# Optimization experiments

Measured on AMD Instinct MI355X. Metric: run time of the kernel, lower is better.

Reference implementation:

```python
import jax, jax.numpy as jnp
import numpy as np

SOFTCAP = 50.0  # GEMMA2_TANH_SCALE
N_HEADS = 16

def _rope(x, cos, sin):
    # x: [B,S,H,D]; cos/sin: [S,D/2]; interleaved complex pairs as in apply_rotary_emb
    x0 = x[..., 0::2]
    x1 = x[..., 1::2]
    c = cos[None, :, None, :]
    s = sin[None, :, None, :]
    r0 = x0 * c - x1 * s
    r1 = x0 * s + x1 * c
    return jnp.stack([r0, r1], axis=-1).reshape(x.shape)

def setup_inputs() -> dict:
    key = jax.random.key(0)
    ks = jax.random.split(key, 5)
    B, S, DM = 1, 2048, 2048
    hd = DM // N_HEADS
    scale = 1.0 / np.sqrt(DM)
    x = jax.random.normal(ks[0], (B, S, DM), jnp.float32)
    wq = jax.random.normal(ks[1], (DM, DM), jnp.float32) * scale
    wk = jax.random.normal(ks[2], (DM, DM), jnp.float32) * scale
    wv = jax.random.normal(ks[3], (DM, DM), jnp.float32) * scale
    wo = jax.random.normal(ks[4], (DM, DM), jnp.float32) * scale
    # rotary tables, theta=10000 as in llama
    inv_freq = 10000.0 ** (-jnp.arange(0, hd, 2, dtype=jnp.float32) / hd)
    ang = jnp.arange(S, dtype=jnp.float32)[:, None] * inv_freq[None, :]
    return {"x": x, "wq": wq, "wk": wk, "wv": wv, "wo": wo,
            "freqs_cos": jnp.cos(ang), "freqs_sin": jnp.sin(ang)}

def reference(x, wq, wk, wv, wo, freqs_cos, freqs_sin):
    B, S, DM = x.shape
    H = N_HEADS
    hd = DM // H
    q = (x @ wq).reshape(B, S, H, hd)
    k = (x @ wk).reshape(B, S, H, hd)
    v = (x @ wv).reshape(B, S, H, hd)
    q = _rope(q, freqs_cos, freqs_sin)
    k = _rope(k, freqs_cos, freqs_sin)
    # scores [B,H,S,S]
    scores = jnp.einsum('bqhd,bkhd->bhqk', q, k) / jnp.sqrt(jnp.float32(hd))
    scores = SOFTCAP * jnp.tanh(scores / SOFTCAP)  # gemma2 tanh soft-cap
    causal = jnp.tril(jnp.ones((S, S), dtype=bool))
    scores = jnp.where(causal[None, None], scores, -jnp.inf)
    p = jax.nn.softmax(scores, axis=-1)
    o = jnp.einsum('bhqk,bkhd->bqhd', p, v).reshape(B, S, DM)
    return o @ wo
```

## Files before the change

### kernel.cpp

```cpp
#include <hip/hip_runtime.h>
#include <hip/hip_bf16.h>

typedef __attribute__((ext_vector_type(8))) short short8;
typedef __attribute__((ext_vector_type(4))) short short4v;
typedef __attribute__((ext_vector_type(4))) float f32x4;
typedef __attribute__((ext_vector_type(4))) float float4v;

#define S_LEN 2048
#define DMODEL 2048
#define N_HEADS 16
#define HEAD_DIM 128

__device__ __forceinline__ float bf2f(__hip_bfloat16 b) { return __bfloat162float(b); }
__device__ __forceinline__ __hip_bfloat16 f2bf(float f) { return __float2bfloat16(f); }
__device__ __forceinline__ short bfs(float f) {
    union { __hip_bfloat16 b; short s; } x; x.b = __float2bfloat16(f); return x.s;
}
__device__ __forceinline__ float sbf(short s) {
    union { short s; __hip_bfloat16 b; } x; x.s = s; return __bfloat162float(x.b);
}

#if __has_builtin(__builtin_amdgcn_global_load_lds)
#define HAVE_ASYNC_LDS 1
#else
#define HAVE_ASYNC_LDS 0
#endif

__device__ __forceinline__ void stage16(const __hip_bfloat16* g, __hip_bfloat16* ldsbase, int lane) {
#if HAVE_ASYNC_LDS
    __builtin_amdgcn_global_load_lds(
        (const __attribute__((address_space(1))) unsigned int*)g,
        (__attribute__((address_space(3))) unsigned int*)ldsbase,
        16, 0, 0);
#else
    *(short8*)((char*)ldsbase + lane * 16) = *(const short8*)g;
#endif
}

__global__ __launch_bounds__(256) void prep(const float* __restrict__ x,
                                            const float* __restrict__ w0,
                                            const float* __restrict__ w1,
                                            const float* __restrict__ w2,
                                            const float* __restrict__ w3,
                                            __hip_bfloat16* __restrict__ xb,
                                            __hip_bfloat16* __restrict__ o0,
                                            __hip_bfloat16* __restrict__ o1,
                                            __hip_bfloat16* __restrict__ o2,
                                            __hip_bfloat16* __restrict__ o3) {
    const int z = blockIdx.z;
    const int tid = threadIdx.x;
    if (z == 4) {
        size_t base = (((size_t)blockIdx.y * 32 + blockIdx.x) * 256 + tid) * 16;
        for (int i = 0; i < 4; ++i) {
            float4v v = *(const float4v*)(x + base + i * 4);
            short4v p;
            p.x = bfs(v.x); p.y = bfs(v.y); p.z = bfs(v.z); p.w = bfs(v.w);
            *(short4v*)((short*)xb + base + i * 4) = p;
        }
        return;
    }
    const float* in = (z == 0) ? w0 : (z == 1) ? w1 : (z == 2) ? w2 : w3;
    __hip_bfloat16* out = (z == 0) ? o0 : (z == 1) ? o1 : (z == 2) ? o2 : o3;
    __shared__ short tile[64][68];
    const int bx = blockIdx.x * 64;
    const int by = blockIdx.y * 64;
    const int c4 = (tid & 15) * 4;
    for (int rr = 0; rr < 4; ++rr) {
        int r = (tid >> 4) + rr * 16;
        float4v v = *(const float4v*)(in + (size_t)(by + r) * DMODEL + bx + c4);
        short4v p;
        p.x = bfs(v.x); p.y = bfs(v.y); p.z = bfs(v.z); p.w = bfs(v.w);
        *(short4v*)&tile[r][c4] = p;
    }
    __syncthreads();
    const int oc = tid >> 2;
    const int s0 = (tid & 3) * 16;
    short8 a, b;
    for (int i = 0; i < 8; ++i) ((short*)&a)[i] = tile[s0 + i][oc];
    for (int i = 0; i < 8; ++i) ((short*)&b)[i] = tile[s0 + 8 + i][oc];
    *(short8*)((short*)out + (size_t)(bx + oc) * DMODEL + by + s0) = a;
    *(short8*)((short*)out + (size_t)(bx + oc) * DMODEL + by + s0 + 8) = b;
}

__global__ __launch_bounds__(256) void gemm_qkv_sk(const __hip_bfloat16* __restrict__ A,
                                                   const __hip_bfloat16* __restrict__ Bq,
                                                   const __hip_bfloat16* __restrict__ Bk,
                                                   const __hip_bfloat16* __restrict__ Bv,
                                                   __hip_bfloat16* __restrict__ Q0,
                                                   __hip_bfloat16* __restrict__ Q1,
                                                   __hip_bfloat16* __restrict__ K0,
                                                   __hip_bfloat16* __restrict__ K1,
                                                   __hip_bfloat16* __restrict__ V0t,
                                                   __hip_bfloat16* __restrict__ V1t) {
    __shared__ alignas(16) __hip_bfloat16 As[128 * 32];
    __shared__ alignas(16) __hip_bfloat16 Bs[128 * 32];
    const int bx = blockIdx.x;
    const int which = bx >> 5;
    const int kh = (bx >> 4) & 1;
    const __hip_bfloat16* Bt = (which == 0) ? Bq : (which == 1) ? Bk : Bv;
    const int tid = threadIdx.x;
    const int wave = tid >> 6;
    const int lane = tid & 63;
    const int lane15 = lane & 15;
    const int quad = lane >> 4;
    const int m0 = blockIdx.y * 128;
    const int n0 = (bx & 15) * 128;
    const int wm = (wave >> 1) * 64;
    const int wn = (wave & 1) * 64;

    f32x4 acc[4][4];
    for (int i = 0; i < 4; ++i)
        for (int j = 0; j < 4; ++j)
            acc[i][j] = {0.f, 0.f, 0.f, 0.f};

    const int rA = lane >> 2;
    const int cA = (lane & 3) * 8;
    const int kbeg = kh * 1024;

    for (int k0 = kbeg; k0 < kbeg + 1024; k0 += 32) {
        __syncthreads();
        for (int c = 0; c < 4; ++c) {
            int chunk = wave * 4 + c;
            if (chunk < 8) {
                int r = chunk * 16 + rA;
                stage16(A + (size_t)(m0 + r) * DMODEL + k0 + cA, As + chunk * 512, lane);
            } else {
                int r = (chunk - 8) * 16 + rA;
                stage16(Bt + (size_t)(n0 + r) * DMODEL + k0 + cA, Bs + (chunk - 8) * 512, lane);
            }
        }
#if HAVE_ASYNC_LDS
        asm volatile("s_waitcnt vmcnt(0)" ::: "memory");
#endif
        __syncthreads();

        short8 af[4], bfr[4];
        for (int mt = 0; mt < 4; ++mt)
            af[mt] = *(const short8*)(As + (wm + mt * 16 + lane15) * 32 + quad * 8);
        for (int nt = 0; nt < 4; ++nt)
            bfr[nt] = *(const short8*)(Bs + (wn + nt * 16 + lane15) * 32 + quad * 8);
        for (int mt = 0; mt < 4; ++mt)
            for (int nt = 0; nt < 4; ++nt)
                acc[mt][nt] = __builtin_amdgcn_mfma_f32_16x16x32_bf16(af[mt], bfr[nt], acc[mt][nt], 0, 0, 0);
    }

    if (which < 2) {
        __hip_bfloat16* C = (which == 0) ? (kh ? Q1 : Q0) : (kh ? K1 : K0);
        for (int mt = 0; mt < 4; ++mt)
            for (int nt = 0; nt < 4; ++nt)
                for (int i = 0; i < 4; ++i) {
                    int row = m0 + wm + mt * 16 + quad * 4 + i;
                    int col = n0 + wn + nt * 16 + lane15;
                    C[(size_t)row * DMODEL + col] = f2bf(acc[mt][nt][i]);
                }
    } else {
        __hip_bfloat16* Vp = kh ? V1t : V0t;
        for (int mt = 0; mt < 4; ++mt) {
            int rowbase = m0 + wm + mt * 16 + quad * 4;
            for (int nt = 0; nt < 4; ++nt) {
                int col = n0 + wn + nt * 16 + lane15;
                short4v pk;
                pk.x = bfs(acc[mt][nt][0]);
                pk.y = bfs(acc[mt][nt][1]);
                pk.z = bfs(acc[mt][nt][2]);
                pk.w = bfs(acc[mt][nt][3]);
                *(short4v*)((short*)Vp + (size_t)col * S_LEN + rowbase) = pk;
            }
        }
    }
}

__global__ __launch_bounds__(256) void reduce_rope(__hip_bfloat16* __restrict__ Q0,
                                                   const __hip_bfloat16* __restrict__ Q1,
                                                   __hip_bfloat16* __restrict__ K0,
                                                   const __hip_bfloat16* __restrict__ K1,
                                                   __hip_bfloat16* __restrict__ V0,
                                                   const __hip_bfloat16* __restrict__ V1,
                                                   const float* __restrict__ fc,
                                                   const float* __restrict__ fs) {
    const int z = blockIdx.z;
    __hip_bfloat16* P0 = (z == 0) ? Q0 : (z == 1) ? K0 : V0;
    const __hip_bfloat16* P1 = (z == 0) ? Q1 : (z == 1) ? K1 : V1;
    size_t i0 = ((size_t)blockIdx.x * 256 + threadIdx.x) * 8;
    short8 a = *(const short8*)((const short*)P0 + i0);
    short8 b = *(const short8*)((const short*)P1 + i0);
    float s[8];
    for (int i = 0; i < 8; ++i) s[i] = sbf(((short*)&a)[i]) + sbf(((short*)&b)[i]);
    short8 o;
    if (z < 2) {
        int row = (int)(i0 >> 11);
        int col = (int)(i0 & 2047);
        int j0 = (col & 127) >> 1;
        for (int p = 0; p < 4; ++p) {
            float c = fc[row * 64 + j0 + p];
            float sn = fs[row * 64 + j0 + p];
            float e = s[2 * p], od = s[2 * p + 1];
            ((short*)&o)[2 * p]     = bfs(e * c - od * sn);
            ((short*)&o)[2 * p + 1] = bfs(e * sn + od * c);
        }
    } else {
        for (int i = 0; i < 8; ++i) ((short*)&o)[i] = bfs(s[i]);
    }
    *(short8*)((short*)P0 + i0) = o;
}

__global__ __launch_bounds__(256) void gemm_qkv_fused(const __hip_bfloat16* __restrict__ A,
                                                      const __hip_bfloat16* __restrict__ Bq,
                                                      const __hip_bfloat16* __restrict__ Bk,
                                                      const __hip_bfloat16* __restrict__ Bv,
                                                      __hip_bfloat16* __restrict__ Cq,
                                                      __hip_bfloat16* __restrict__ Ck,
                                                      __hip_bfloat16* __restrict__ Cvt,
                                                      const float* __restrict__ fc,
                                                      const float* __restrict__ fs) {
    __shared__ alignas(16) __hip_bfloat16 As[2][128 * 32];
    __shared__ alignas(16) __hip_bfloat16 Bs[2][128 * 32];
    const int which = blockIdx.x >> 4;
    const __hip_bfloat16* Bt = (which == 0) ? Bq : (which == 1) ? Bk : Bv;
    const int tid = threadIdx.x;
    const int wave = tid >> 6;
    const int lane = tid & 63;
    const int lane15 = lane & 15;
    const int quad = lane >> 4;
    const int m0 = blockIdx.y * 128;
    const int n0 = (blockIdx.x & 15) * 128;
    const int wm = (wave >> 1) * 64;
    const int wn = (wave & 1) * 64;
    f32x4 acc[4][4];
    for (int i = 0; i < 4; ++i)
        for (int j = 0; j < 4; ++j)
            acc[i][j] = {0.f, 0.f, 0.f, 0.f};
    const int rA = lane >> 2;
    const int cA = (lane & 3) * 8;
    for (int k0 = 0; k0 < DMODEL; k0 += 64) {
        __syncthreads();
        for (int h = 0; h < 2; ++h) {
            int kk = k0 + h * 32;
            for (int c = 0; c < 4; ++c) {
                int chunk = wave * 4 + c;
                if (chunk < 8) {
                    int r = chunk * 16 + rA;
                    stage16(A + (size_t)(m0 + r) * DMODEL + kk + cA, As[h] + chunk * 512, lane);
                } else {
                    int r = (chunk - 8) * 16 + rA;
                    stage16(Bt + (size_t)(n0 + r) * DMODEL + kk + cA, Bs[h] + (chunk - 8) * 512, lane);
                }
            }
        }
#if HAVE_ASYNC_LDS
        asm volatile("s_waitcnt vmcnt(0)" ::: "memory");
#endif
        __syncthreads();
        for (int h = 0; h < 2; ++h) {
            short8 af[4], bfr[4];
            for (int mt = 0; mt < 4; ++mt)
                af[mt] = *(const short8*)(As[h] + (wm + mt * 16 + lane15) * 32 + quad * 8);
            for (int nt = 0; nt < 4; ++nt)
                bfr[nt] = *(const short8*)(Bs[h] + (wn + nt * 16 + lane15) * 32 + quad * 8);
            for (int mt = 0; mt < 4; ++mt)
                for (int nt = 0; nt < 4; ++nt)
                    acc[mt][nt] = __builtin_amdgcn_mfma_f32_16x16x32_bf16(af[mt], bfr[nt], acc[mt][nt], 0, 0, 0);
        }
    }
    if (which < 2) {
        __hip_bfloat16* C = (which == 0) ? Cq : Ck;
        for (int mt = 0; mt < 4; ++mt)
            for (int nt = 0; nt < 4; ++nt) {
                int col = n0 + wn + nt * 16 + lane15;
                int j = (col & 127) >> 1;
                bool odd = col & 1;
                for (int i = 0; i < 4; ++i) {
                    int row = m0 + wm + mt * 16 + quad * 4 + i;
                    float v = acc[mt][nt][i];
                    float p = __shfl_xor(v, 1, 64);
                    float c = fc[row * 64 + j];
                    float sn = fs[row * 64 + j];
                    float r = odd ? (p * sn + v * c) : (v * c - p * sn);
                    C[(size_t)row * DMODEL + col] = f2bf(r);
                }
            }
    } else {
        for (int mt = 0; mt < 4; ++mt) {
            int rowbase = m0 + wm + mt * 16 + quad * 4;
            for (int nt = 0; nt < 4; ++nt) {
                int col = n0 + wn + nt * 16 + lane15;
                short4v pk;
                pk.x = bfs(acc[mt][nt][0]);
                pk.y = bfs(acc[mt][nt][1]);
                pk.z = bfs(acc[mt][nt][2]);
                pk.w = bfs(acc[mt][nt][3]);
                *(short4v*)((short*)Cvt + (size_t)col * S_LEN + rowbase) = pk;
            }
        }
    }
}

__global__ __launch_bounds__(256) void gemm_out(const __hip_bfloat16* __restrict__ A,
                                                const __hip_bfloat16* __restrict__ Bt,
                                                float* __restrict__ C) {
    __shared__ alignas(16) __hip_bfloat16 As[2][128 * 32];
    __shared__ alignas(16) __hip_bfloat16 Bs[2][64 * 32];
    const int tid = threadIdx.x;
    const int wave = tid >> 6;
    const int lane = tid & 63;
    const int lane15 = lane & 15;
    const int quad = lane >> 4;
    const int m0 = blockIdx.y * 128;
    const int n0 = blockIdx.x * 64;
    const int wm = (wave >> 1) * 64;
    const int wn = (wave & 1) * 32;
    f32x4 acc[4][2];
    for (int i = 0; i < 4; ++i)
        for (int j = 0; j < 2; ++j)
            acc[i][j] = {0.f, 0.f, 0.f, 0.f};
    const int rA = lane >> 2;
    const int cA = (lane & 3) * 8;
    for (int k0 = 0; k0 < DMODEL; k0 += 64) {
        __syncthreads();
        for (int h = 0; h < 2; ++h) {
            int kk = k0 + h * 32;
            for (int c = 0; c < 3; ++c) {
                int chunk = wave * 3 + c;
                if (chunk < 8) {
                    int r = chunk * 16 + rA;
                    stage16(A + (size_t)(m0 + r) * DMODEL + kk + cA, As[h] + chunk * 512, lane);
                } else {
                    int r = (chunk - 8) * 16 + rA;
                    stage16(Bt + (size_t)(n0 + r) * DMODEL + kk + cA, Bs[h] + (chunk - 8) * 512, lane);
                }
            }
        }
#if HAVE_ASYNC_LDS
        asm volatile("s_waitcnt vmcnt(0)" ::: "memory");
#endif
        __syncthreads();
        for (int h = 0; h < 2; ++h) {
            short8 af[4], bfr[2];
            for (int mt = 0; mt < 4; ++mt)
                af[mt] = *(const short8*)(As[h] + (wm + mt * 16 + lane15) * 32 + quad * 8);
            for (int nt = 0; nt < 2; ++nt)
                bfr[nt] = *(const short8*)(Bs[h] + (wn + nt * 16 + lane15) * 32 + quad * 8);
            for (int mt = 0; mt < 4; ++mt)
                for (int nt = 0; nt < 2; ++nt)
                    acc[mt][nt] = __builtin_amdgcn_mfma_f32_16x16x32_bf16(af[mt], bfr[nt], acc[mt][nt], 0, 0, 0);
        }
    }
    for (int mt = 0; mt < 4; ++mt)
        for (int nt = 0; nt < 2; ++nt)
            for (int i = 0; i < 4; ++i) {
                int row = m0 + wm + mt * 16 + quad * 4 + i;
                int col = n0 + wn + nt * 16 + lane15;
                C[(size_t)row * DMODEL + col] = acc[mt][nt][i];
            }
}

__global__ __launch_bounds__(256) void flash_attn(const __hip_bfloat16* __restrict__ Q,
                                                  const __hip_bfloat16* __restrict__ Kb,
                                                  const __hip_bfloat16* __restrict__ Vt,
                                                  __hip_bfloat16* __restrict__ O) {
    __shared__ alignas(16) short Ks[32][136];
    __shared__ alignas(16) short Vs[128][40];
    __shared__ alignas(16) short Pl[4][16][40];
    const int tid = threadIdx.x;
    const int wave = tid >> 6;
    const int lane = tid & 63;
    const int lane15 = lane & 15;
    const int quad = lane >> 4;
    const int bx = blockIdx.x;
    const int u = bx & 255;
    const int head = u & 15;
    const int qp = u >> 4;
    const int qb = (bx < 256) ? (31 - qp) : qp;
    const int qbase = qb * 64;
    const int q0w = qbase + wave * 16;
    const int nkt = 2 * qb + 2;
    const float K1 = 0.08838834764831845f * (1.0f / 25.0f);

    const __hip_bfloat16* Qh = Q + (size_t)q0w * DMODEL + head * HEAD_DIM;
    short8 qf[4];
    for (int kk = 0; kk < 4; ++kk)
        qf[kk] = *(const short8*)(Qh + (size_t)lane15 * DMODEL + kk * 32 + quad * 8);

    f32x4 acc[8];
    for (int i = 0; i < 8; ++i) acc[i] = {0.f, 0.f, 0.f, 0.f};
    float lpart[4] = {0.f, 0.f, 0.f, 0.f};

    const int krow = tid >> 3, kcol = (tid & 7) * 16;
    const int vrow = tid >> 1, vcol = (tid & 1) * 16;
    const __hip_bfloat16* Kg = Kb + (size_t)krow * DMODEL + head * HEAD_DIM + kcol;
    const __hip_bfloat16* Vg = Vt + (size_t)(head * HEAD_DIM + vrow) * S_LEN + vcol;

    short8 gk0 = *(const short8*)(Kg);
    short8 gk1 = *(const short8*)(Kg + 8);
    short8 gv0 = *(const short8*)(Vg);
    short8 gv1 = *(const short8*)(Vg + 8);

    for (int kt = 0; kt < nkt; ++kt) {
        const int kb = kt * 32;
        __syncthreads();
        *(short8*)&Ks[krow][kcol] = gk0;
        *(short8*)&Ks[krow][kcol + 8] = gk1;
        *(short8*)&Vs[vrow][vcol] = gv0;
        *(short8*)&Vs[vrow][vcol + 8] = gv1;
        __syncthreads();

        if (kt + 1 < nkt) {
            const __hip_bfloat16* Kg2 = Kg + (size_t)(kb + 32) * DMODEL;
            const __hip_bfloat16* Vg2 = Vg + kb + 32;
            gk0 = *(const short8*)(Kg2);
            gk1 = *(const short8*)(Kg2 + 8);
            gv0 = *(const short8*)(Vg2);
            gv1 = *(const short8*)(Vg2 + 8);
        }

        if (kb <= q0w + 15) {
            f32x4 sc[2];
            sc[0] = {0.f, 0.f, 0.f, 0.f};
            sc[1] = {0.f, 0.f, 0.f, 0.f};
            for (int c = 0; c < 2; ++c)
                for (int kk = 0; kk < 4; ++kk) {
                    short8 kf = *(const short8*)&Ks[c * 16 + lane15][kk * 32 + quad * 8];
                    sc[c] = __builtin_amdgcn_mfma_f32_16x16x32_bf16(qf[kk], kf, sc[c], 0, 0, 0);
                }

            const bool masked = (kb + 31 > q0w);
            const int key0 = kb + lane15;
            const int key1 = kb + 16 + lane15;
            for (int i = 0; i < 4; ++i) {
                float e0 = __expf(sc[0][i] * K1);
                float e1 = __expf(sc[1][i] * K1);
                float c0 = __builtin_fmaf(-100.0f, __builtin_amdgcn_rcpf(e0 + 1.0f), 40.0f);
                float c1 = __builtin_fmaf(-100.0f, __builtin_amdgcn_rcpf(e1 + 1.0f), 40.0f);
                float p0 = __expf(c0);
                float p1 = __expf(c1);
                if (masked) {
                    int q = q0w + quad * 4 + i;
                    if (key0 > q) p0 = 0.f;
                    if (key1 > q) p1 = 0.f;
                }
                short b0 = bfs(p0), b1 = bfs(p1);
                lpart[i] += sbf(b0) + sbf(b1);
                Pl[wave][quad * 4 + i][lane15] = b0;
                Pl[wave][quad * 4 + i][16 + lane15] = b1;
            }
            asm volatile("s_waitcnt lgkmcnt(0)" ::: "memory");
            short8 pf = *(const short8*)&Pl[wave][lane15][quad * 8];
            asm volatile("" ::: "memory");
            for (int nt = 0; nt < 8; ++nt) {
                short8 vf = *(const short8*)&Vs[nt * 16 + lane15][quad * 8];
                acc[nt] = __builtin_amdgcn_mfma_f32_16x16x32_bf16(pf, vf, acc[nt], 0, 0, 0);
            }
        }
    }

    for (int i = 0; i < 4; ++i) {
        float l = lpart[i];
        l += __shfl_xor(l, 1, 64);
        l += __shfl_xor(l, 2, 64);
        l += __shfl_xor(l, 4, 64);
        l += __shfl_xor(l, 8, 64);
        float inv = 1.0f / l;
        int row = q0w + quad * 4 + i;
        for (int nt = 0; nt < 8; ++nt) {
            int col = head * HEAD_DIM + nt * 16 + lane15;
            O[(size_t)row * DMODEL + col] = f2bf(acc[nt][i] * inv);
        }
    }
}

extern "C" void kernel_launch(void* const* d_in, const int* in_sizes, int n_in,
                              void* d_out, int out_size, void* d_ws, size_t ws_size,
                              hipStream_t stream) {
    const float* x  = (const float*)d_in[0];
    const float* wq = (const float*)d_in[1];
    const float* wk = (const float*)d_in[2];
    const float* wv = (const float*)d_in[3];
    const float* wo = (const float*)d_in[4];
    const float* fc = (const float*)d_in[5];
    const float* fs = (const float*)d_in[6];
    float* out = (float*)d_out;

    char* ws = (char*)d_ws;
    const size_t MB8 = (size_t)2048 * 2048 * sizeof(__hip_bfloat16);
    __hip_bfloat16* wq_t = (__hip_bfloat16*)(ws + 0 * MB8);
    __hip_bfloat16* wk_t = (__hip_bfloat16*)(ws + 1 * MB8);
    __hip_bfloat16* wv_t = (__hip_bfloat16*)(ws + 2 * MB8);
    __hip_bfloat16* wo_t = (__hip_bfloat16*)(ws + 3 * MB8);
    __hip_bfloat16* s4   = (__hip_bfloat16*)(ws + 4 * MB8);
    __hip_bfloat16* s5   = (__hip_bfloat16*)(ws + 5 * MB8);
    __hip_bfloat16* s6   = (__hip_bfloat16*)(ws + 6 * MB8);
    __hip_bfloat16* s7   = (__hip_bfloat16*)(ws + 7 * MB8);
    __hip_bfloat16* s8   = (__hip_bfloat16*)(ws + 8 * MB8);
    __hip_bfloat16* s9   = (__hip_bfloat16*)(ws + 9 * MB8);
    __hip_bfloat16* x_bf = (__hip_bfloat16*)d_out;

    prep<<<dim3(32, 32, 5), 256, 0, stream>>>(x, wq, wk, wv, wo, x_bf, wq_t, wk_t, wv_t, wo_t);

    if (ws_size >= 10 * MB8) {
        gemm_qkv_sk<<<dim3(96, 16), 256, 0, stream>>>(x_bf, wq_t, wk_t, wv_t,
                                                      s4, s7, s5, s8, s6, s9);
        reduce_rope<<<dim3(2048, 1, 3), 256, 0, stream>>>(s4, s7, s5, s8, s6, s9, fc, fs);
        flash_attn<<<512, 256, 0, stream>>>(s4, s5, s6, wq_t);
        gemm_out<<<dim3(32, 16), 256, 0, stream>>>(wq_t, wo_t, out);
    } else {
        gemm_qkv_fused<<<dim3(48, 16), 256, 0, stream>>>(x_bf, wq_t, wk_t, wv_t,
                                                         s4, s5, s6, fc, fs);
        flash_attn<<<512, 256, 0, stream>>>(s4, s5, s6, wq_t);
        gemm_out<<<dim3(32, 16), 256, 0, stream>>>(wq_t, wo_t, out);
    }
}
```

Measured before the change: 306.5 us.

## Replace split-K QKV GEMM with 256x256 eight-wave pipelined GEMM fusing RoPE

Replaces the split-K QKV projection and its separate reduce+RoPE kernel with a single 256x256-tile, 512-thread GEMM. It double-buffers 64-wide K tiles in a 128KB swizzled LDS and interleaves async global-to-LDS staging with MFMA phases, using barriers and raised wave priority. RoPE and the V transpose are applied in the epilogue. This removes the partial-sum round trip through memory and one kernel launch, and gives more reuse per tile. The cost is only 192 blocks, which is fewer than the CU count, and heavy register and LDS pressure.

```diff
diff --git a/kernel.cpp b/kernel.cpp
--- a/kernel.cpp
+++ b/kernel.cpp
@@ -10,6 +10,7 @@
 #define DMODEL 2048
 #define N_HEADS 16
 #define HEAD_DIM 128
+#define NKT 32
 
 __device__ __forceinline__ float bf2f(__hip_bfloat16 b) { return __bfloat162float(b); }
 __device__ __forceinline__ __hip_bfloat16 f2bf(float f) { return __float2bfloat16(f); }
@@ -82,195 +83,158 @@
     *(short8*)((short*)out + (size_t)(bx + oc) * DMODEL + by + s0 + 8) = b;
 }
 
-__global__ __launch_bounds__(256) void gemm_qkv_sk(const __hip_bfloat16* __restrict__ A,
-                                                   const __hip_bfloat16* __restrict__ Bq,
-                                                   const __hip_bfloat16* __restrict__ Bk,
-                                                   const __hip_bfloat16* __restrict__ Bv,
-                                                   __hip_bfloat16* __restrict__ Q0,
-                                                   __hip_bfloat16* __restrict__ Q1,
-                                                   __hip_bfloat16* __restrict__ K0,
-                                                   __hip_bfloat16* __restrict__ K1,
-                                                   __hip_bfloat16* __restrict__ V0t,
-                                                   __hip_bfloat16* __restrict__ V1t) {
-    __shared__ alignas(16) __hip_bfloat16 As[128 * 32];
-    __shared__ alignas(16) __hip_bfloat16 Bs[128 * 32];
-    const int bx = blockIdx.x;
-    const int which = bx >> 5;
-    const int kh = (bx >> 4) & 1;
-    const __hip_bfloat16* Bt = (which == 0) ? Bq : (which == 1) ? Bk : Bv;
+
+#define CFENCE asm volatile("" ::: "memory")
+#define BARRIER do { CFENCE; __builtin_amdgcn_s_barrier(); CFENCE; } while (0)
+#define WAIT_LGKM0 asm volatile("s_waitcnt lgkmcnt(0)" ::: "memory")
+#define WAIT_VM(n) asm volatile("s_waitcnt vmcnt(" #n ")" ::: "memory")
+
+
+#define STAGE_A8(buf, half, kt) do {                                                        \
+    const __hip_bfloat16* gpA_ = A + (size_t)(m0 + (half) * 128 + wave * 16 + rsel) * DMODEL \
+                                 + (kt) * 64 + gsrc;                                        \
+    __hip_bfloat16* lpA_ = (__hip_bfloat16*)(smem + ((buf) * 2 + (half)) * 8192 + wave * 1024); \
+    stage16(gpA_, lpA_, lane);                                                              \
+    stage16(gpA_ + (size_t)8 * DMODEL, lpA_ + 512, lane);                                   \
+} while (0)
+
+#define STAGE_B8(buf, half, kt) do {                                                        \
+    const __hip_bfloat16* gpB_ = Bt + (size_t)(n0 + (half) * 128 + wave * 16 + rsel) * DMODEL \
+                                 + (kt) * 64 + gsrc;                                        \
+    __hip_bfloat16* lpB_ = (__hip_bfloat16*)(smem + 32768 + ((buf) * 2 + (half)) * 8192 + wave * 1024); \
+    stage16(gpB_, lpB_, lane);                                                              \
+    stage16(gpB_ + (size_t)8 * DMODEL, lpB_ + 512, lane);                                   \
+} while (0)
+
+#define LDA4(buf, mb) do {                                                                  \
+    const char* ab_ = (const char*)(smem + ((buf) * 2 + wr) * 8192);                        \
+    _Pragma("unroll")                                                                       \
+    for (int mt_ = 0; mt_ < 4; ++mt_) {                                                     \
+        const int rowL_ = ((mb) + mt_) * 16 + lane15;                                       \
+        const int r7_ = rowL_ & 7;                                                          \
+        af[(mb) + mt_][0] = *(const short8*)(ab_ + rowL_ * 128 + ((quad ^ r7_) * 16));      \
+        af[(mb) + mt_][1] = *(const short8*)(ab_ + rowL_ * 128 + (((4 + quad) ^ r7_) * 16));\
+    }                                                                                       \
+} while (0)
+
+#define LDB2(buf, nb) do {                                                                  \
+    const char* bb_ = (const char*)(smem + 32768 + ((buf) * 2 + hb) * 8192);                \
+    _Pragma("unroll")                                                                       \
+    for (int nt_ = 0; nt_ < 2; ++nt_) {                                                     \
+        const int rowL_ = wc1 * 64 + ((nb) + nt_) * 16 + lane15;                            \
+        const int r7_ = rowL_ & 7;                                                          \
+        bfr[nt_][0] = *(const short8*)(bb_ + rowL_ * 128 + ((quad ^ r7_) * 16));            \
+        bfr[nt_][1] = *(const short8*)(bb_ + rowL_ * 128 + (((4 + quad) ^ r7_) * 16));      \
+    }                                                                                       \
+} while (0)
+
+#define MFMAQ(mb, nb) do {                                                                  \
+    _Pragma("unroll")                                                                       \
+    for (int mt_ = 0; mt_ < 4; ++mt_) {                                                     \
+        _Pragma("unroll")                                                                   \
+        for (int nt_ = 0; nt_ < 2; ++nt_) {                                                 \
+            acc[(mb) + mt_][(nb) + nt_] = __builtin_amdgcn_mfma_f32_16x16x32_bf16(          \
+                af[(mb) + mt_][0], bfr[nt_][0], acc[(mb) + mt_][(nb) + nt_], 0, 0, 0);      \
+            acc[(mb) + mt_][(nb) + nt_] = __builtin_amdgcn_mfma_f32_16x16x32_bf16(          \
+                af[(mb) + mt_][1], bfr[nt_][1], acc[(mb) + mt_][(nb) + nt_], 0, 0, 0);      \
+        }                                                                                   \
+    }                                                                                       \
+} while (0)
+
+#define GROUP(g, cur, nxt) do {                                                             \
+    const int g_ = (g);                                                                     \
+    const bool stB_ = (g_ + 1 < NKT);                                                       \
+    const bool stA_ = (g_ + 2 < NKT);                                                       \
+                                                     \
+    LDA4(cur, 0); LDB2(cur, 0);                                                             \
+    if (stB_) STAGE_B8(nxt, 0, g_ + 1);                                                     \
+    BARRIER; WAIT_LGKM0;                                                                    \
+    __builtin_amdgcn_s_setprio(1); MFMAQ(0, 0); __builtin_amdgcn_s_setprio(0);              \
+    BARRIER;                                                                                \
+                                                                \
+    LDA4(cur, 4);                                                                           \
+    if (stB_) STAGE_B8(nxt, 1, g_ + 1);                                                     \
+    BARRIER; WAIT_LGKM0;                                                                    \
+    __builtin_amdgcn_s_setprio(1); MFMAQ(4, 0); __builtin_amdgcn_s_setprio(0);              \
+    BARRIER;                                                                                \
+                                                                \
+    LDB2(cur, 2);                                                                           \
+    if (stA_) STAGE_A8(cur, 0, g_ + 2);                                                     \
+    BARRIER; WAIT_LGKM0;                                                                    \
+    __builtin_amdgcn_s_setprio(1); MFMAQ(0, 2); __builtin_amdgcn_s_setprio(0);              \
+    BARRIER;                                                                                \
+                                                                \
+    if (stA_) STAGE_A8(cur, 1, g_ + 2);                                                     \
+    BARRIER;                                                                                \
+    __builtin_amdgcn_s_setprio(1); MFMAQ(4, 2); __builtin_amdgcn_s_setprio(0);              \
+    if (stA_) { WAIT_VM(4); } else if (stB_) { WAIT_VM(0); }                                \
+    BARRIER;                                                                                \
+} while (0)
+
+__global__ __launch_bounds__(512, 2) void gemm_qkv_8ph(const __hip_bfloat16* __restrict__ A,
+                                                       const __hip_bfloat16* __restrict__ Bq,
+                                                       const __hip_bfloat16* __restrict__ Bk,
+                                                       const __hip_bfloat16* __restrict__ Bv,
+                                                       __hip_bfloat16* __restrict__ Cq,
+                                                       __hip_bfloat16* __restrict__ Ck,
+                                                       __hip_bfloat16* __restrict__ Cvt,
+                                                       const float* __restrict__ fc,
+                                                       const float* __restrict__ fs) {
+    __shared__ alignas(16) short smem[65536];
+
     const int tid = threadIdx.x;
     const int wave = tid >> 6;
     const int lane = tid & 63;
     const int lane15 = lane & 15;
     const int quad = lane >> 4;
-    const int m0 = blockIdx.y * 128;
-    const int n0 = (bx & 15) * 128;
-    const int wm = (wave >> 1) * 64;
-    const int wn = (wave & 1) * 64;
-
-    f32x4 acc[4][4];
-    for (int i = 0; i < 4; ++i)
+    const int wr = wave >> 2;
+    const int wc = wave & 3;
+    const int wc1 = wc & 1;
+    const int hb = wc >> 1;
+    const int rsel = lane >> 3;
+    const int gsrc = ((lane & 7) ^ rsel) * 8;
+
+    const int which = blockIdx.x >> 3;
+    const int n0 = (blockIdx.x & 7) * 256;
+    const int m0 = blockIdx.y * 256;
+    const __hip_bfloat16* Bt = (which == 0) ? Bq : (which == 1) ? Bk : Bv;
+
+    short8 af[8][2];
+    short8 bfr[2][2];
+    f32x4 acc[8][4];
+
+    STAGE_A8(0, 0, 0);
+    STAGE_B8(0, 0, 0);
+    STAGE_A8(0, 1, 0);
+    STAGE_B8(0, 1, 0);
+    STAGE_A8(1, 0, 1);
+    STAGE_A8(1, 1, 1);
+#pragma unroll
+    for (int i = 0; i < 8; ++i)
+#pragma unroll
         for (int j = 0; j < 4; ++j)
             acc[i][j] = {0.f, 0.f, 0.f, 0.f};
-
-    const int rA = lane >> 2;
-    const int cA = (lane & 3) * 8;
-    const int kbeg = kh * 1024;
-
-    for (int k0 = kbeg; k0 < kbeg + 1024; k0 += 32) {
-        __syncthreads();
-        for (int c = 0; c < 4; ++c) {
-            int chunk = wave * 4 + c;
-            if (chunk < 8) {
-                int r = chunk * 16 + rA;
-                stage16(A + (size_t)(m0 + r) * DMODEL + k0 + cA, As + chunk * 512, lane);
-            } else {
-                int r = (chunk - 8) * 16 + rA;
-                stage16(Bt + (size_t)(n0 + r) * DMODEL + k0 + cA, Bs + (chunk - 8) * 512, lane);
-            }
-        }
-#if HAVE_ASYNC_LDS
-        asm volatile("s_waitcnt vmcnt(0)" ::: "memory");
-#endif
-        __syncthreads();
-
-        short8 af[4], bfr[4];
-        for (int mt = 0; mt < 4; ++mt)
-            af[mt] = *(const short8*)(As + (wm + mt * 16 + lane15) * 32 + quad * 8);
-        for (int nt = 0; nt < 4; ++nt)
-            bfr[nt] = *(const short8*)(Bs + (wn + nt * 16 + lane15) * 32 + quad * 8);
-        for (int mt = 0; mt < 4; ++mt)
-            for (int nt = 0; nt < 4; ++nt)
-                acc[mt][nt] = __builtin_amdgcn_mfma_f32_16x16x32_bf16(af[mt], bfr[nt], acc[mt][nt], 0, 0, 0);
-    }
-
-    if (which < 2) {
-        __hip_bfloat16* C = (which == 0) ? (kh ? Q1 : Q0) : (kh ? K1 : K0);
-        for (int mt = 0; mt < 4; ++mt)
-            for (int nt = 0; nt < 4; ++nt)
-                for (int i = 0; i < 4; ++i) {
-                    int row = m0 + wm + mt * 16 + quad * 4 + i;
-                    int col = n0 + wn + nt * 16 + lane15;
-                    C[(size_t)row * DMODEL + col] = f2bf(acc[mt][nt][i]);
-                }
-    } else {
-        __hip_bfloat16* Vp = kh ? V1t : V0t;
-        for (int mt = 0; mt < 4; ++mt) {
-            int rowbase = m0 + wm + mt * 16 + quad * 4;
-            for (int nt = 0; nt < 4; ++nt) {
-                int col = n0 + wn + nt * 16 + lane15;
-                short4v pk;
-                pk.x = bfs(acc[mt][nt][0]);
-                pk.y = bfs(acc[mt][nt][1]);
-                pk.z = bfs(acc[mt][nt][2]);
-                pk.w = bfs(acc[mt][nt][3]);
-                *(short4v*)((short*)Vp + (size_t)col * S_LEN + rowbase) = pk;
-            }
-        }
-    }
-}
-
-__global__ __launch_bounds__(256) void reduce_rope(__hip_bfloat16* __restrict__ Q0,
-                                                   const __hip_bfloat16* __restrict__ Q1,
-                                                   __hip_bfloat16* __restrict__ K0,
-                                                   const __hip_bfloat16* __restrict__ K1,
-                                                   __hip_bfloat16* __restrict__ V0,
-                                                   const __hip_bfloat16* __restrict__ V1,
-                                                   const float* __restrict__ fc,
-                                                   const float* __restrict__ fs) {
-    const int z = blockIdx.z;
-    __hip_bfloat16* P0 = (z == 0) ? Q0 : (z == 1) ? K0 : V0;
-    const __hip_bfloat16* P1 = (z == 0) ? Q1 : (z == 1) ? K1 : V1;
-    size_t i0 = ((size_t)blockIdx.x * 256 + threadIdx.x) * 8;
-    short8 a = *(const short8*)((const short*)P0 + i0);
-    short8 b = *(const short8*)((const short*)P1 + i0);
-    float s[8];
-    for (int i = 0; i < 8; ++i) s[i] = sbf(((short*)&a)[i]) + sbf(((short*)&b)[i]);
-    short8 o;
-    if (z < 2) {
-        int row = (int)(i0 >> 11);
-        int col = (int)(i0 & 2047);
-        int j0 = (col & 127) >> 1;
-        for (int p = 0; p < 4; ++p) {
-            float c = fc[row * 64 + j0 + p];
-            float sn = fs[row * 64 + j0 + p];
-            float e = s[2 * p], od = s[2 * p + 1];
-            ((short*)&o)[2 * p]     = bfs(e * c - od * sn);
-            ((short*)&o)[2 * p + 1] = bfs(e * sn + od * c);
-        }
-    } else {
-        for (int i = 0; i < 8; ++i) ((short*)&o)[i] = bfs(s[i]);
-    }
-    *(short8*)((short*)P0 + i0) = o;
-}
-
-__global__ __launch_bounds__(256) void gemm_qkv_fused(const __hip_bfloat16* __restrict__ A,
-                                                      const __hip_bfloat16* __restrict__ Bq,
-                                                      const __hip_bfloat16* __restrict__ Bk,
-                                                      const __hip_bfloat16* __restrict__ Bv,
-                                                      __hip_bfloat16* __restrict__ Cq,
-                                                      __hip_bfloat16* __restrict__ Ck,
-                                                      __hip_bfloat16* __restrict__ Cvt,
-                                                      const float* __restrict__ fc,
-                                                      const float* __restrict__ fs) {
-    __shared__ alignas(16) __hip_bfloat16 As[2][128 * 32];
-    __shared__ alignas(16) __hip_bfloat16 Bs[2][128 * 32];
-    const int which = blockIdx.x >> 4;
-    const __hip_bfloat16* Bt = (which == 0) ? Bq : (which == 1) ? Bk : Bv;
-    const int tid = threadIdx.x;
-    const int wave = tid >> 6;
-    const int lane = tid & 63;
-    const int lane15 = lane & 15;
-    const int quad = lane >> 4;
-    const int m0 = blockIdx.y * 128;
-    const int n0 = (blockIdx.x & 15) * 128;
-    const int wm = (wave >> 1) * 64;
-    const int wn = (wave & 1) * 64;
-    f32x4 acc[4][4];
-    for (int i = 0; i < 4; ++i)
-        for (int j = 0; j < 4; ++j)
-            acc[i][j] = {0.f, 0.f, 0.f, 0.f};
-    const int rA = lane >> 2;
-    const int cA = (lane & 3) * 8;
-    for (int k0 = 0; k0 < DMODEL; k0 += 64) {
-        __syncthreads();
-        for (int h = 0; h < 2; ++h) {
-            int kk = k0 + h * 32;
-            for (int c = 0; c < 4; ++c) {
-                int chunk = wave * 4 + c;
-                if (chunk < 8) {
-                    int r = chunk * 16 + rA;
-                    stage16(A + (size_t)(m0 + r) * DMODEL + kk + cA, As[h] + chunk * 512, lane);
-                } else {
-                    int r = (chunk - 8) * 16 + rA;
-                    stage16(Bt + (size_t)(n0 + r) * DMODEL + kk + cA, Bs[h] + (chunk - 8) * 512, lane);
-                }
-            }
-        }
-#if HAVE_ASYNC_LDS
-        asm volatile("s_waitcnt vmcnt(0)" ::: "memory");
-#endif
-        __syncthreads();
-        for (int h = 0; h < 2; ++h) {
-            short8 af[4], bfr[4];
-            for (int mt = 0; mt < 4; ++mt)
-                af[mt] = *(const short8*)(As[h] + (wm + mt * 16 + lane15) * 32 + quad * 8);
-            for (int nt = 0; nt < 4; ++nt)
-                bfr[nt] = *(const short8*)(Bs[h] + (wn + nt * 16 + lane15) * 32 + quad * 8);
-            for (int mt = 0; mt < 4; ++mt)
-                for (int nt = 0; nt < 4; ++nt)
-                    acc[mt][nt] = __builtin_amdgcn_mfma_f32_16x16x32_bf16(af[mt], bfr[nt], acc[mt][nt], 0, 0, 0);
-        }
-    }
+    WAIT_VM(4);
+    BARRIER;
+
+#pragma unroll 1
+    for (int g = 0; g < NKT; g += 2) {
+        GROUP(g, 0, 1);
+        GROUP(g + 1, 1, 0);
+    }
+
     if (which < 2) {
         __hip_bfloat16* C = (which == 0) ? Cq : Ck;
-        for (int mt = 0; mt < 4; ++mt)
+#pragma unroll
+        for (int mt = 0; mt < 8; ++mt)
+#pragma unroll
             for (int nt = 0; nt < 4; ++nt) {
-                int col = n0 + wn + nt * 16 + lane15;
+                int col = n0 + wc * 64 + nt * 16 + lane15;
                 int j = (col & 127) >> 1;
                 bool odd = col & 1;
+#pragma unroll
                 for (int i = 0; i < 4; ++i) {
-                    int row = m0 + wm + mt * 16 + quad * 4 + i;
+                    int row = m0 + wr * 128 + mt * 16 + quad * 4 + i;
                     float v = acc[mt][nt][i];
                     float p = __shfl_xor(v, 1, 64);
                     float c = fc[row * 64 + j];
@@ -280,10 +244,12 @@
                 }
             }
     } else {
-        for (int mt = 0; mt < 4; ++mt) {
-            int rowbase = m0 + wm + mt * 16 + quad * 4;
+#pragma unroll
+        for (int mt = 0; mt < 8; ++mt) {
+            int rowbase = m0 + wr * 128 + mt * 16 + quad * 4;
+#pragma unroll
             for (int nt = 0; nt < 4; ++nt) {
-                int col = n0 + wn + nt * 16 + lane15;
+                int col = n0 + wc * 64 + nt * 16 + lane15;
                 short4v pk;
                 pk.x = bfs(acc[mt][nt][0]);
                 pk.y = bfs(acc[mt][nt][1]);
@@ -489,23 +455,12 @@
     __hip_bfloat16* s4   = (__hip_bfloat16*)(ws + 4 * MB8);
     __hip_bfloat16* s5   = (__hip_bfloat16*)(ws + 5 * MB8);
     __hip_bfloat16* s6   = (__hip_bfloat16*)(ws + 6 * MB8);
-    __hip_bfloat16* s7   = (__hip_bfloat16*)(ws + 7 * MB8);
-    __hip_bfloat16* s8   = (__hip_bfloat16*)(ws + 8 * MB8);
-    __hip_bfloat16* s9   = (__hip_bfloat16*)(ws + 9 * MB8);
     __hip_bfloat16* x_bf = (__hip_bfloat16*)d_out;
 
     prep<<<dim3(32, 32, 5), 256, 0, stream>>>(x, wq, wk, wv, wo, x_bf, wq_t, wk_t, wv_t, wo_t);
 
-    if (ws_size >= 10 * MB8) {
-        gemm_qkv_sk<<<dim3(96, 16), 256, 0, stream>>>(x_bf, wq_t, wk_t, wv_t,
-                                                      s4, s7, s5, s8, s6, s9);
-        reduce_rope<<<dim3(2048, 1, 3), 256, 0, stream>>>(s4, s7, s5, s8, s6, s9, fc, fs);
-        flash_attn<<<512, 256, 0, stream>>>(s4, s5, s6, wq_t);
-        gemm_out<<<dim3(32, 16), 256, 0, stream>>>(wq_t, wo_t, out);
-    } else {
-        gemm_qkv_fused<<<dim3(48, 16), 256, 0, stream>>>(x_bf, wq_t, wk_t, wv_t,
-                                                         s4, s5, s6, fc, fs);
-        flash_attn<<<512, 256, 0, stream>>>(s4, s5, s6, wq_t);
-        gemm_out<<<dim3(32, 16), 256, 0, stream>>>(wq_t, wo_t, out);
-    }
-}
+    gemm_qkv_8ph<<<dim3(24, 8), 512, 0, stream>>>(x_bf, wq_t, wk_t, wv_t, s4, s5, s6, fc, fs);
+
+    flash_attn<<<512, 256, 0, stream>>>(s4, s5, s6, wq_t);
+    gemm_out<<<dim3(32, 16), 256, 0, stream>>>(wq_t, wo_t, out);
+}
```

After: 298.2 us. -2.7%, faster.

## Split attention KV range across two blocks and fuse combine into output GEMM

Applied to the files above, without the earlier changes.

Flash attention now launches twice as many blocks, each handling half of a query block's causal KV range. Each block writes unnormalized fp32 partial outputs and row sums instead of normalized bf16 output. The output GEMM reads both partials, adds them, normalizes by the summed row sums, converts to bf16 while staging its A tile, then multiplies as before. This is meant to fix load imbalance and low occupancy in causal attention. The QKV step also drops its split-K GEMM plus reduce/RoPE pass in favour of the single fused QKV GEMM. The trade-off is much more fp32 traffic in the output GEMM's A loads, and the partial sums are only valid because the softcap bounds the scores so no running-max rescaling is needed.

```diff
diff --git a/kernel.cpp b/kernel.cpp
--- a/kernel.cpp
+++ b/kernel.cpp
@@ -80,128 +80,6 @@
     for (int i = 0; i < 8; ++i) ((short*)&b)[i] = tile[s0 + 8 + i][oc];
     *(short8*)((short*)out + (size_t)(bx + oc) * DMODEL + by + s0) = a;
     *(short8*)((short*)out + (size_t)(bx + oc) * DMODEL + by + s0 + 8) = b;
-}
-
-__global__ __launch_bounds__(256) void gemm_qkv_sk(const __hip_bfloat16* __restrict__ A,
-                                                   const __hip_bfloat16* __restrict__ Bq,
-                                                   const __hip_bfloat16* __restrict__ Bk,
-                                                   const __hip_bfloat16* __restrict__ Bv,
-                                                   __hip_bfloat16* __restrict__ Q0,
-                                                   __hip_bfloat16* __restrict__ Q1,
-                                                   __hip_bfloat16* __restrict__ K0,
-                                                   __hip_bfloat16* __restrict__ K1,
-                                                   __hip_bfloat16* __restrict__ V0t,
-                                                   __hip_bfloat16* __restrict__ V1t) {
-    __shared__ alignas(16) __hip_bfloat16 As[128 * 32];
-    __shared__ alignas(16) __hip_bfloat16 Bs[128 * 32];
-    const int bx = blockIdx.x;
-    const int which = bx >> 5;
-    const int kh = (bx >> 4) & 1;
-    const __hip_bfloat16* Bt = (which == 0) ? Bq : (which == 1) ? Bk : Bv;
-    const int tid = threadIdx.x;
-    const int wave = tid >> 6;
-    const int lane = tid & 63;
-    const int lane15 = lane & 15;
-    const int quad = lane >> 4;
-    const int m0 = blockIdx.y * 128;
-    const int n0 = (bx & 15) * 128;
-    const int wm = (wave >> 1) * 64;
-    const int wn = (wave & 1) * 64;
-
-    f32x4 acc[4][4];
-    for (int i = 0; i < 4; ++i)
-        for (int j = 0; j < 4; ++j)
-            acc[i][j] = {0.f, 0.f, 0.f, 0.f};
-
-    const int rA = lane >> 2;
-    const int cA = (lane & 3) * 8;
-    const int kbeg = kh * 1024;
-
-    for (int k0 = kbeg; k0 < kbeg + 1024; k0 += 32) {
-        __syncthreads();
-        for (int c = 0; c < 4; ++c) {
-            int chunk = wave * 4 + c;
-            if (chunk < 8) {
-                int r = chunk * 16 + rA;
-                stage16(A + (size_t)(m0 + r) * DMODEL + k0 + cA, As + chunk * 512, lane);
-            } else {
-                int r = (chunk - 8) * 16 + rA;
-                stage16(Bt + (size_t)(n0 + r) * DMODEL + k0 + cA, Bs + (chunk - 8) * 512, lane);
-            }
-        }
-#if HAVE_ASYNC_LDS
-        asm volatile("s_waitcnt vmcnt(0)" ::: "memory");
-#endif
-        __syncthreads();
-
-        short8 af[4], bfr[4];
-        for (int mt = 0; mt < 4; ++mt)
-            af[mt] = *(const short8*)(As + (wm + mt * 16 + lane15) * 32 + quad * 8);
-        for (int nt = 0; nt < 4; ++nt)
-            bfr[nt] = *(const short8*)(Bs + (wn + nt * 16 + lane15) * 32 + quad * 8);
-        for (int mt = 0; mt < 4; ++mt)
-            for (int nt = 0; nt < 4; ++nt)
-                acc[mt][nt] = __builtin_amdgcn_mfma_f32_16x16x32_bf16(af[mt], bfr[nt], acc[mt][nt], 0, 0, 0);
-    }
-
-    if (which < 2) {
-        __hip_bfloat16* C = (which == 0) ? (kh ? Q1 : Q0) : (kh ? K1 : K0);
-        for (int mt = 0; mt < 4; ++mt)
-            for (int nt = 0; nt < 4; ++nt)
-                for (int i = 0; i < 4; ++i) {
-                    int row = m0 + wm + mt * 16 + quad * 4 + i;
-                    int col = n0 + wn + nt * 16 + lane15;
-                    C[(size_t)row * DMODEL + col] = f2bf(acc[mt][nt][i]);
-                }
-    } else {
-        __hip_bfloat16* Vp = kh ? V1t : V0t;
-        for (int mt = 0; mt < 4; ++mt) {
-            int rowbase = m0 + wm + mt * 16 + quad * 4;
-            for (int nt = 0; nt < 4; ++nt) {
-                int col = n0 + wn + nt * 16 + lane15;
-                short4v pk;
-                pk.x = bfs(acc[mt][nt][0]);
-                pk.y = bfs(acc[mt][nt][1]);
-                pk.z = bfs(acc[mt][nt][2]);
-                pk.w = bfs(acc[mt][nt][3]);
-                *(short4v*)((short*)Vp + (size_t)col * S_LEN + rowbase) = pk;
-            }
-        }
-    }
-}
-
-__global__ __launch_bounds__(256) void reduce_rope(__hip_bfloat16* __restrict__ Q0,
-                                                   const __hip_bfloat16* __restrict__ Q1,
-                                                   __hip_bfloat16* __restrict__ K0,
-                                                   const __hip_bfloat16* __restrict__ K1,
-                                                   __hip_bfloat16* __restrict__ V0,
-                                                   const __hip_bfloat16* __restrict__ V1,
-                                                   const float* __restrict__ fc,
-                                                   const float* __restrict__ fs) {
-    const int z = blockIdx.z;
-    __hip_bfloat16* P0 = (z == 0) ? Q0 : (z == 1) ? K0 : V0;
-    const __hip_bfloat16* P1 = (z == 0) ? Q1 : (z == 1) ? K1 : V1;
-    size_t i0 = ((size_t)blockIdx.x * 256 + threadIdx.x) * 8;
-    short8 a = *(const short8*)((const short*)P0 + i0);
-    short8 b = *(const short8*)((const short*)P1 + i0);
-    float s[8];
-    for (int i = 0; i < 8; ++i) s[i] = sbf(((short*)&a)[i]) + sbf(((short*)&b)[i]);
-    short8 o;
-    if (z < 2) {
-        int row = (int)(i0 >> 11);
-        int col = (int)(i0 & 2047);
-        int j0 = (col & 127) >> 1;
-        for (int p = 0; p < 4; ++p) {
-            float c = fc[row * 64 + j0 + p];
-            float sn = fs[row * 64 + j0 + p];
-            float e = s[2 * p], od = s[2 * p + 1];
-            ((short*)&o)[2 * p]     = bfs(e * c - od * sn);
-            ((short*)&o)[2 * p + 1] = bfs(e * sn + od * c);
-        }
-    } else {
-        for (int i = 0; i < 8; ++i) ((short*)&o)[i] = bfs(s[i]);
-    }
-    *(short8*)((short*)P0 + i0) = o;
 }
 
 __global__ __launch_bounds__(256) void gemm_qkv_fused(const __hip_bfloat16* __restrict__ A,
@@ -295,69 +173,13 @@
     }
 }
 
-__global__ __launch_bounds__(256) void gemm_out(const __hip_bfloat16* __restrict__ A,
-                                                const __hip_bfloat16* __restrict__ Bt,
-                                                float* __restrict__ C) {
-    __shared__ alignas(16) __hip_bfloat16 As[2][128 * 32];
-    __shared__ alignas(16) __hip_bfloat16 Bs[2][64 * 32];
-    const int tid = threadIdx.x;
-    const int wave = tid >> 6;
-    const int lane = tid & 63;
-    const int lane15 = lane & 15;
-    const int quad = lane >> 4;
-    const int m0 = blockIdx.y * 128;
-    const int n0 = blockIdx.x * 64;
-    const int wm = (wave >> 1) * 64;
-    const int wn = (wave & 1) * 32;
-    f32x4 acc[4][2];
-    for (int i = 0; i < 4; ++i)
-        for (int j = 0; j < 2; ++j)
-            acc[i][j] = {0.f, 0.f, 0.f, 0.f};
-    const int rA = lane >> 2;
-    const int cA = (lane & 3) * 8;
-    for (int k0 = 0; k0 < DMODEL; k0 += 64) {
-        __syncthreads();
-        for (int h = 0; h < 2; ++h) {
-            int kk = k0 + h * 32;
-            for (int c = 0; c < 3; ++c) {
-                int chunk = wave * 3 + c;
-                if (chunk < 8) {
-                    int r = chunk * 16 + rA;
-                    stage16(A + (size_t)(m0 + r) * DMODEL + kk + cA, As[h] + chunk * 512, lane);
-                } else {
-                    int r = (chunk - 8) * 16 + rA;
-                    stage16(Bt + (size_t)(n0 + r) * DMODEL + kk + cA, Bs[h] + (chunk - 8) * 512, lane);
-                }
-            }
-        }
-#if HAVE_ASYNC_LDS
-        asm volatile("s_waitcnt vmcnt(0)" ::: "memory");
-#endif
-        __syncthreads();
-        for (int h = 0; h < 2; ++h) {
-            short8 af[4], bfr[2];
-            for (int mt = 0; mt < 4; ++mt)
-                af[mt] = *(const short8*)(As[h] + (wm + mt * 16 + lane15) * 32 + quad * 8);
-            for (int nt = 0; nt < 2; ++nt)
-                bfr[nt] = *(const short8*)(Bs[h] + (wn + nt * 16 + lane15) * 32 + quad * 8);
-            for (int mt = 0; mt < 4; ++mt)
-                for (int nt = 0; nt < 2; ++nt)
-                    acc[mt][nt] = __builtin_amdgcn_mfma_f32_16x16x32_bf16(af[mt], bfr[nt], acc[mt][nt], 0, 0, 0);
-        }
-    }
-    for (int mt = 0; mt < 4; ++mt)
-        for (int nt = 0; nt < 2; ++nt)
-            for (int i = 0; i < 4; ++i) {
-                int row = m0 + wm + mt * 16 + quad * 4 + i;
-                int col = n0 + wn + nt * 16 + lane15;
-                C[(size_t)row * DMODEL + col] = acc[mt][nt][i];
-            }
-}
-
 __global__ __launch_bounds__(256) void flash_attn(const __hip_bfloat16* __restrict__ Q,
                                                   const __hip_bfloat16* __restrict__ Kb,
                                                   const __hip_bfloat16* __restrict__ Vt,
-                                                  __hip_bfloat16* __restrict__ O) {
+                                                  float* __restrict__ N0,
+                                                  float* __restrict__ N1,
+                                                  float* __restrict__ L0,
+                                                  float* __restrict__ L1) {
     __shared__ alignas(16) short Ks[32][136];
     __shared__ alignas(16) short Vs[128][40];
     __shared__ alignas(16) short Pl[4][16][40];
@@ -367,14 +189,19 @@
     const int lane15 = lane & 15;
     const int quad = lane >> 4;
     const int bx = blockIdx.x;
-    const int u = bx & 255;
+    const int chunk = bx >> 9;
+    const int bxl = bx & 511;
+    const int u = bxl & 255;
     const int head = u & 15;
     const int qp = u >> 4;
-    const int qb = (bx < 256) ? (31 - qp) : qp;
-    const int qbase = qb * 64;
-    const int q0w = qbase + wave * 16;
-    const int nkt = 2 * qb + 2;
+    const int qb = (bxl < 256) ? (31 - qp) : qp;
+    const int q0w = qb * 64 + wave * 16;
+    const int k_lo = chunk ? (qb + 1) : 0;
+    const int k_hi = chunk ? (2 * qb + 2) : (qb + 1);
     const float K1 = 0.08838834764831845f * (1.0f / 25.0f);
+
+    float* __restrict__ Nw = chunk ? N1 : N0;
+    float* __restrict__ Lw = chunk ? L1 : L0;
 
     const __hip_bfloat16* Qh = Q + (size_t)q0w * DMODEL + head * HEAD_DIM;
     short8 qf[4];
@@ -390,12 +217,13 @@
     const __hip_bfloat16* Kg = Kb + (size_t)krow * DMODEL + head * HEAD_DIM + kcol;
     const __hip_bfloat16* Vg = Vt + (size_t)(head * HEAD_DIM + vrow) * S_LEN + vcol;
 
-    short8 gk0 = *(const short8*)(Kg);
-    short8 gk1 = *(const short8*)(Kg + 8);
-    short8 gv0 = *(const short8*)(Vg);
-    short8 gv1 = *(const short8*)(Vg + 8);
-
-    for (int kt = 0; kt < nkt; ++kt) {
+    const int kb0 = k_lo * 32;
+    short8 gk0 = *(const short8*)(Kg + (size_t)kb0 * DMODEL);
+    short8 gk1 = *(const short8*)(Kg + (size_t)kb0 * DMODEL + 8);
+    short8 gv0 = *(const short8*)(Vg + kb0);
+    short8 gv1 = *(const short8*)(Vg + kb0 + 8);
+
+    for (int kt = k_lo; kt < k_hi; ++kt) {
         const int kb = kt * 32;
         __syncthreads();
         *(short8*)&Ks[krow][kcol] = gk0;
@@ -404,7 +232,7 @@
         *(short8*)&Vs[vrow][vcol + 8] = gv1;
         __syncthreads();
 
-        if (kt + 1 < nkt) {
+        if (kt + 1 < k_hi) {
             const __hip_bfloat16* Kg2 = Kg + (size_t)(kb + 32) * DMODEL;
             const __hip_bfloat16* Vg2 = Vg + kb + 32;
             gk0 = *(const short8*)(Kg2);
@@ -459,13 +287,94 @@
         l += __shfl_xor(l, 2, 64);
         l += __shfl_xor(l, 4, 64);
         l += __shfl_xor(l, 8, 64);
-        float inv = 1.0f / l;
         int row = q0w + quad * 4 + i;
+        if (lane15 == 0) Lw[(head << 11) + row] = l;
         for (int nt = 0; nt < 8; ++nt) {
             int col = head * HEAD_DIM + nt * 16 + lane15;
-            O[(size_t)row * DMODEL + col] = f2bf(acc[nt][i] * inv);
-        }
-    }
+            Nw[(size_t)row * DMODEL + col] = acc[nt][i];
+        }
+    }
+}
+
+__global__ __launch_bounds__(256) void gemm_out_fused(const float* __restrict__ N0,
+                                                      const float* __restrict__ N1,
+                                                      const float* __restrict__ L0,
+                                                      const float* __restrict__ L1,
+                                                      const __hip_bfloat16* __restrict__ Bt,
+                                                      float* __restrict__ C) {
+    __shared__ alignas(16) __hip_bfloat16 As[2][128 * 32];
+    __shared__ alignas(16) __hip_bfloat16 Bs[2][64 * 32];
+    const int tid = threadIdx.x;
+    const int wave = tid >> 6;
+    const int lane = tid & 63;
+    const int lane15 = lane & 15;
+    const int quad = lane >> 4;
+    const int m0 = blockIdx.y * 128;
+    const int n0 = blockIdx.x * 64;
+    const int wm = (wave >> 1) * 64;
+    const int wn = (wave & 1) * 32;
+    f32x4 acc[4][2];
+    for (int i = 0; i < 4; ++i)
+        for (int j = 0; j < 2; ++j)
+            acc[i][j] = {0.f, 0.f, 0.f, 0.f};
+    const int rA = lane >> 2;
+    const int cA = (lane & 3) * 8;
+    for (int k0 = 0; k0 < DMODEL; k0 += 64) {
+        __syncthreads();
+        for (int h = 0; h < 2; ++h) {
+            int kk = k0 + h * 32;
+            for (int c = 0; c < 3; ++c) {
+                int chunk = wave * 3 + c;
+                if (chunk < 8) {
+                    int row = m0 + chunk * 16 + rA;
+                    int colb = kk + cA;
+                    int head = colb >> 7;
+                    float l = L0[(head << 11) + row] + L1[(head << 11) + row];
+                    float inv = __builtin_amdgcn_rcpf(l);
+                    const float* p0 = N0 + (size_t)row * DMODEL + colb;
+                    const float* p1 = N1 + (size_t)row * DMODEL + colb;
+                    float4v a0 = *(const float4v*)p0;
+                    float4v b0 = *(const float4v*)(p0 + 4);
+                    float4v a1 = *(const float4v*)p1;
+                    float4v b1 = *(const float4v*)(p1 + 4);
+                    short8 pk;
+                    ((short*)&pk)[0] = bfs((a0.x + a1.x) * inv);
+                    ((short*)&pk)[1] = bfs((a0.y + a1.y) * inv);
+                    ((short*)&pk)[2] = bfs((a0.z + a1.z) * inv);
+                    ((short*)&pk)[3] = bfs((a0.w + a1.w) * inv);
+                    ((short*)&pk)[4] = bfs((b0.x + b1.x) * inv);
+                    ((short*)&pk)[5] = bfs((b0.y + b1.y) * inv);
+                    ((short*)&pk)[6] = bfs((b0.z + b1.z) * inv);
+                    ((short*)&pk)[7] = bfs((b0.w + b1.w) * inv);
+                    *(short8*)((char*)(As[h] + chunk * 512) + lane * 16) = pk;
+                } else {
+                    int r = (chunk - 8) * 16 + rA;
+                    stage16(Bt + (size_t)(n0 + r) * DMODEL + kk + cA, Bs[h] + (chunk - 8) * 512, lane);
+                }
+            }
+        }
+#if HAVE_ASYNC_LDS
+        asm volatile("s_waitcnt vmcnt(0)" ::: "memory");
+#endif
+        __syncthreads();
+        for (int h = 0; h < 2; ++h) {
+            short8 af[4], bfr[2];
+            for (int mt = 0; mt < 4; ++mt)
+                af[mt] = *(const short8*)(As[h] + (wm + mt * 16 + lane15) * 32 + quad * 8);
+            for (int nt = 0; nt < 2; ++nt)
+                bfr[nt] = *(const short8*)(Bs[h] + (wn + nt * 16 + lane15) * 32 + quad * 8);
+            for (int mt = 0; mt < 4; ++mt)
+                for (int nt = 0; nt < 2; ++nt)
+                    acc[mt][nt] = __builtin_amdgcn_mfma_f32_16x16x32_bf16(af[mt], bfr[nt], acc[mt][nt], 0, 0, 0);
+        }
+    }
+    for (int mt = 0; mt < 4; ++mt)
+        for (int nt = 0; nt < 2; ++nt)
+            for (int i = 0; i < 4; ++i) {
+                int row = m0 + wm + mt * 16 + quad * 4 + i;
+                int col = n0 + wn + nt * 16 + lane15;
+                C[(size_t)row * DMODEL + col] = acc[mt][nt][i];
+            }
 }
 
 extern "C" void kernel_launch(void* const* d_in, const int* in_sizes, int n_in,
@@ -489,23 +398,17 @@
     __hip_bfloat16* s4   = (__hip_bfloat16*)(ws + 4 * MB8);
     __hip_bfloat16* s5   = (__hip_bfloat16*)(ws + 5 * MB8);
     __hip_bfloat16* s6   = (__hip_bfloat16*)(ws + 6 * MB8);
-    __hip_bfloat16* s7   = (__hip_bfloat16*)(ws + 7 * MB8);
-    __hip_bfloat16* s8   = (__hip_bfloat16*)(ws + 8 * MB8);
-    __hip_bfloat16* s9   = (__hip_bfloat16*)(ws + 9 * MB8);
+    float* N0 = (float*)(ws + 0 * MB8);
+    float* N1 = (float*)(ws + 7 * MB8);
+    float* L0 = (float*)(ws + 9 * MB8);
+    float* L1 = L0 + 2048 * 16;
     __hip_bfloat16* x_bf = (__hip_bfloat16*)d_out;
 
     prep<<<dim3(32, 32, 5), 256, 0, stream>>>(x, wq, wk, wv, wo, x_bf, wq_t, wk_t, wv_t, wo_t);
 
-    if (ws_size >= 10 * MB8) {
-        gemm_qkv_sk<<<dim3(96, 16), 256, 0, stream>>>(x_bf, wq_t, wk_t, wv_t,
-                                                      s4, s7, s5, s8, s6, s9);
-        reduce_rope<<<dim3(2048, 1, 3), 256, 0, stream>>>(s4, s7, s5, s8, s6, s9, fc, fs);
-        flash_attn<<<512, 256, 0, stream>>>(s4, s5, s6, wq_t);
-        gemm_out<<<dim3(32, 16), 256, 0, stream>>>(wq_t, wo_t, out);
-    } else {
-        gemm_qkv_fused<<<dim3(48, 16), 256, 0, stream>>>(x_bf, wq_t, wk_t, wv_t,
-                                                         s4, s5, s6, fc, fs);
-        flash_attn<<<512, 256, 0, stream>>>(s4, s5, s6, wq_t);
-        gemm_out<<<dim3(32, 16), 256, 0, stream>>>(wq_t, wo_t, out);
-    }
-}
+    gemm_qkv_fused<<<dim3(48, 16), 256, 0, stream>>>(x_bf, wq_t, wk_t, wv_t, s4, s5, s6, fc, fs);
+
+    flash_attn<<<1024, 256, 0, stream>>>(s4, s5, s6, N0, N1, L0, L1);
+
+    gemm_out_fused<<<dim3(32, 16), 256, 0, stream>>>(N0, N1, L0, L1, wo_t, out);
+}
```

New measurement: 349.6 us. +14.0%, slower.
